# Performance work log

Hardware: AMD Instinct MI355X
Metric: run time of the kernel (lower is better)

Reference implementation:

```python
import jax, jax.numpy as jnp
import numpy as np

K = 128        # numClass
PUW = 1.0      # puW from __init__
EPS = 0.01     # the +0.01 clamp inside log(1 - p + 0.01)


def setup_inputs() -> dict:
    key = jax.random.key(0)
    k1, k2, k3 = jax.random.split(key, 3)
    N = 262144
    outputs = jax.random.normal(k1, (N, K), dtype=jnp.float32)
    # labels in [0, K]; label == K means 'unlabeled' (goes to U set)
    labels = jax.random.randint(k2, (N,), 0, K + 1, dtype=jnp.int64)
    priorlist = jax.random.uniform(k3, (K,), dtype=jnp.float32)
    indexlist = jnp.arange(32, dtype=jnp.int64)  # the 32 labeled classes
    return {"outputs": outputs, "labels": labels,
            "priorlist": priorlist, "indexlist": indexlist}


def reference(outputs, labels, priorlist, indexlist):
    outputs = outputs.astype(jnp.float32)
    s = jax.nn.softmax(outputs, axis=1)                      # [N, K]

    maskP = (labels <= K - 1)                                # positive (labeled)
    maskU = jnp.logical_not(maskP)                           # unlabeled
    fP = maskP.astype(jnp.float32)
    fU = maskU.astype(jnp.float32)
    nP = jnp.maximum(jnp.float32(1.0), fP.sum())
    nU = jnp.maximum(jnp.float32(1.0), fU.sum())

    neglog = -jnp.log(1.0 - s + EPS)                         # [N, K]
    sumU = jnp.sum(neglog * fU[:, None], axis=0)             # [K] sums over U rows
    sumP = jnp.sum(neglog * fP[:, None], axis=0)             # [K] sums over P rows

    L = indexlist.shape[0]
    in_idx = jnp.zeros((K,), dtype=bool).at[indexlist].set(True)

    # classes in indexlist: pu3; classes not in indexlist: pu1
    pu3 = jnp.sum(jnp.where(in_idx, sumU, 0.0)) / nU / L
    pu1 = (jnp.sum(jnp.where(in_idx, 0.0, sumP))
           * priorlist[indexlist[0]] / nP / (K - L))

    # pu2: per positive sample, -log(1 - p[label] + eps) * prior[label]
    lab_c = jnp.clip(labels, 0, K - 1)
    gathered = jnp.take_along_axis(neglog, lab_c[:, None], axis=1)[:, 0]
    pu2 = jnp.sum(gathered * priorlist[lab_c] * fP) / nP

    PULoss = pu3 + pu1 - pu2

    # mean cross-entropy over positive samples only
    logp = jax.nn.log_softmax(outputs, axis=1)
    ce_per = -jnp.take_along_axis(logp, lab_c[:, None], axis=1)[:, 0]
    crossloss = jnp.sum(ce_per * fP) / nP

    objective = crossloss
    return (objective, PULoss * PUW, crossloss)
```

## Files before the change

kernel.cpp:

```cpp
#include <hip/hip_runtime.h>
#include <math.h>

#define KCLS 128

__global__ __launch_bounds__(256) void pu_main(
    const float* __restrict__ outp, const int* __restrict__ labels,
    const int* __restrict__ idxlist, const float* __restrict__ prior,
    double* __restrict__ acc, int N, int L)
{
    __shared__ __align__(16) float s_notin[KCLS];
    __shared__ __align__(16) float s_prior[KCLS];
    const int tid = threadIdx.x;
    if (tid < KCLS) { s_prior[tid] = prior[tid]; s_notin[tid] = 1.0f; }
    __syncthreads();
    if (tid < L) s_notin[idxlist[tid]] = 0.0f;
    __syncthreads();

    const int lane  = tid & 63;
    const int wave  = tid >> 6;
    const int half  = lane >> 5;
    const int hlane = lane & 31;
    const int globalWave = blockIdx.x * (blockDim.x >> 6) + wave;
    const int numWaves   = gridDim.x * (blockDim.x >> 6);

    const float4 nm4 = ((const float4*)s_notin)[hlane];
    const float4 in4 = make_float4(1.f - nm4.x, 1.f - nm4.y,
                                   1.f - nm4.z, 1.f - nm4.w);
    const float4 pr4 = ((const float4*)s_prior)[hlane];

    float aU = 0.f, aP = 0.f, aPu2 = 0.f, aCE = 0.f, cP = 0.f, cU = 0.f;

    const int npairs = (N + 1) >> 1;
    for (int pair = globalWave; pair < npairs; pair += numWaves) {
        const int row   = pair * 2 + half;
        const bool valid = (row < N);
        const int  rl    = valid ? row : (N - 1);

        const float4 o4 = ((const float4*)(outp + (size_t)rl * KCLS))[hlane];
        const int  lab  = labels[rl];
        const bool isP  = (lab < KCLS);
        const int  labc = isP ? lab : (KCLS - 1);

        const float e0 = __expf(o4.x), e1 = __expf(o4.y),
                    e2 = __expf(o4.z), e3 = __expf(o4.w);
        float psum = (e0 + e1) + (e2 + e3);
        #pragma unroll
        for (int off = 16; off; off >>= 1)
            psum += __shfl_xor(psum, off);
        const float inv = __builtin_amdgcn_rcpf(psum);

        const float s0 = e0 * inv, s1 = e1 * inv, s2 = e2 * inv, s3 = e3 * inv;
        const float nl0 = -__logf((1.0f - s0) + 0.01f);
        const float nl1 = -__logf((1.0f - s1) + 0.01f);
        const float nl2 = -__logf((1.0f - s2) + 0.01f);
        const float nl3 = -__logf((1.0f - s3) + 0.01f);

        const float vP = (valid && isP)  ? 1.f : 0.f;
        const float vU = (valid && !isP) ? 1.f : 0.f;

        aP += vP * ((nl0 * nm4.x + nl1 * nm4.y) + (nl2 * nm4.z + nl3 * nm4.w));
        aU += vU * ((nl0 * in4.x + nl1 * in4.y) + (nl2 * in4.z + nl3 * in4.w));

        if ((labc >> 2) == hlane) {
            const int sub = labc & 3;
            const float olab = (sub == 0) ? o4.x : (sub == 1) ? o4.y : (sub == 2) ? o4.z : o4.w;
            const float nll  = (sub == 0) ? nl0  : (sub == 1) ? nl1  : (sub == 2) ? nl2  : nl3;
            const float prl  = (sub == 0) ? pr4.x : (sub == 1) ? pr4.y : (sub == 2) ? pr4.z : pr4.w;
            aPu2 += vP * nll * prl;
            aCE  += vP * (__logf(psum) - olab);
        }
        if (hlane == 0) { cP += vP; cU += vU; }
    }

    #pragma unroll
    for (int off = 32; off; off >>= 1) {
        aU   += __shfl_xor(aU, off);
        aP   += __shfl_xor(aP, off);
        aPu2 += __shfl_xor(aPu2, off);
        aCE  += __shfl_xor(aCE, off);
        cP   += __shfl_xor(cP, off);
        cU   += __shfl_xor(cU, off);
    }

    __shared__ float s_red[4][6];
    if (lane == 0) {
        s_red[wave][0] = aU;  s_red[wave][1] = aP;   s_red[wave][2] = aPu2;
        s_red[wave][3] = aCE; s_red[wave][4] = cP;   s_red[wave][5] = cU;
    }
    __syncthreads();
    if (tid < 6) {
        float t = 0.f;
        const int nw = blockDim.x >> 6;
        for (int w = 0; w < nw; ++w) t += s_red[w][tid];
        atomicAdd(&acc[tid * 8], (double)t);
    }
}

__global__ void pu_final(const double* __restrict__ acc,
                         const float* __restrict__ prior,
                         const int* __restrict__ idxlist,
                         float* __restrict__ out, int L)
{
    const double aU   = acc[0 * 8];
    const double aP   = acc[1 * 8];
    const double aPu2 = acc[2 * 8];
    const double aCE  = acc[3 * 8];
    const double cP   = acc[4 * 8];
    const double cU   = acc[5 * 8];
    const double nP = cP > 1.0 ? cP : 1.0;
    const double nU = cU > 1.0 ? cU : 1.0;

    const double pu3 = aU / nU / (double)L;
    const double pu1 = aP * (double)prior[idxlist[0]] / nP / (double)(KCLS - L);
    const double pu2 = aPu2 / nP;
    const double ce  = aCE / nP;

    out[0] = (float)ce;
    out[1] = (float)(pu3 + pu1 - pu2);
    out[2] = (float)ce;
}

extern "C" void kernel_launch(void* const* d_in, const int* in_sizes, int n_in,
                              void* d_out, int out_size, void* d_ws, size_t ws_size,
                              hipStream_t stream)
{
    const float* outp   = (const float*)d_in[0];
    const int*   labels = (const int*)d_in[1];
    const float* prior  = (const float*)d_in[2];
    const int*   idxl   = (const int*)d_in[3];
    const int N = in_sizes[1];
    const int L = in_sizes[3];

    double* acc = (double*)d_ws;
    hipMemsetAsync(d_ws, 0, 48 * sizeof(double), stream);

    pu_main<<<1024, 256, 0, stream>>>(outp, labels, idxl, prior, acc, N, L);
    pu_final<<<1, 1, 0, stream>>>(acc, prior, idxl, (float*)d_out, L);
}
```

Measured before the change: 213.6 us.

## Unroll row loop by two and replace double atomics with per-block partials

```diff
diff --git a/kernel.cpp b/kernel.cpp
--- a/kernel.cpp
+++ b/kernel.cpp
@@ -2,11 +2,13 @@
 #include <math.h>
 
 #define KCLS 128
+#define NBLK 1024
+
 
 __global__ __launch_bounds__(256) void pu_main(
     const float* __restrict__ outp, const int* __restrict__ labels,
     const int* __restrict__ idxlist, const float* __restrict__ prior,
-    double* __restrict__ acc, int N, int L)
+    float* __restrict__ part, int N, int L)
 {
     __shared__ __align__(16) float s_notin[KCLS];
     __shared__ __align__(16) float s_prior[KCLS];
@@ -21,7 +23,7 @@
     const int half  = lane >> 5;
     const int hlane = lane & 31;
     const int globalWave = blockIdx.x * (blockDim.x >> 6) + wave;
-    const int numWaves   = gridDim.x * (blockDim.x >> 6);
+    const int numWaves   = NBLK * (256 >> 6);
 
     const float4 nm4 = ((const float4*)s_notin)[hlane];
     const float4 in4 = make_float4(1.f - nm4.x, 1.f - nm4.y,
@@ -30,14 +32,7 @@
 
     float aU = 0.f, aP = 0.f, aPu2 = 0.f, aCE = 0.f, cP = 0.f, cU = 0.f;
 
-    const int npairs = (N + 1) >> 1;
-    for (int pair = globalWave; pair < npairs; pair += numWaves) {
-        const int row   = pair * 2 + half;
-        const bool valid = (row < N);
-        const int  rl    = valid ? row : (N - 1);
-
-        const float4 o4 = ((const float4*)(outp + (size_t)rl * KCLS))[hlane];
-        const int  lab  = labels[rl];
+    auto process = [&](float4 o4, int lab) {
         const bool isP  = (lab < KCLS);
         const int  labc = isP ? lab : (KCLS - 1);
 
@@ -55,8 +50,8 @@
         const float nl2 = -__logf((1.0f - s2) + 0.01f);
         const float nl3 = -__logf((1.0f - s3) + 0.01f);
 
-        const float vP = (valid && isP)  ? 1.f : 0.f;
-        const float vU = (valid && !isP) ? 1.f : 0.f;
+        const float vP = isP ? 1.f : 0.f;
+        const float vU = 1.f - vP;
 
         aP += vP * ((nl0 * nm4.x + nl1 * nm4.y) + (nl2 * nm4.z + nl3 * nm4.w));
         aU += vU * ((nl0 * in4.x + nl1 * in4.y) + (nl2 * in4.z + nl3 * in4.w));
@@ -70,6 +65,24 @@
             aCE  += vP * (__logf(psum) - olab);
         }
         if (hlane == 0) { cP += vP; cU += vU; }
+    };
+
+    const int npairs = N >> 1;
+    int pair = globalWave;
+    for (; pair + numWaves < npairs; pair += 2 * numWaves) {
+        const int rowA = pair * 2 + half;
+        const int rowB = (pair + numWaves) * 2 + half;
+        const float4 oA = ((const float4*)(outp + (size_t)rowA * KCLS))[hlane];
+        const int    lA = labels[rowA];
+        const float4 oB = ((const float4*)(outp + (size_t)rowB * KCLS))[hlane];
+        const int    lB = labels[rowB];
+        process(oA, lA);
+        process(oB, lB);
+    }
+    for (; pair < npairs; pair += numWaves) {
+        const int row = pair * 2 + half;
+        const float4 o = ((const float4*)(outp + (size_t)row * KCLS))[hlane];
+        process(o, labels[row]);
     }
 
     #pragma unroll
@@ -89,35 +102,54 @@
     }
     __syncthreads();
     if (tid < 6) {
-        float t = 0.f;
-        const int nw = blockDim.x >> 6;
-        for (int w = 0; w < nw; ++w) t += s_red[w][tid];
-        atomicAdd(&acc[tid * 8], (double)t);
+        float t = s_red[0][tid] + s_red[1][tid] + s_red[2][tid] + s_red[3][tid];
+        part[tid * NBLK + blockIdx.x] = t;
     }
 }
 
-__global__ void pu_final(const double* __restrict__ acc,
-                         const float* __restrict__ prior,
-                         const int* __restrict__ idxlist,
-                         float* __restrict__ out, int L)
+__global__ __launch_bounds__(256) void pu_final(
+    const float* __restrict__ part, const float* __restrict__ prior,
+    const int* __restrict__ idxlist, float* __restrict__ out, int L)
 {
-    const double aU   = acc[0 * 8];
-    const double aP   = acc[1 * 8];
-    const double aPu2 = acc[2 * 8];
-    const double aCE  = acc[3 * 8];
-    const double cP   = acc[4 * 8];
-    const double cU   = acc[5 * 8];
-    const double nP = cP > 1.0 ? cP : 1.0;
-    const double nU = cU > 1.0 ? cU : 1.0;
+    const int tid  = threadIdx.x;
+    const int lane = tid & 63;
+    const int wave = tid >> 6;
 
-    const double pu3 = aU / nU / (double)L;
-    const double pu1 = aP * (double)prior[idxlist[0]] / nP / (double)(KCLS - L);
-    const double pu2 = aPu2 / nP;
-    const double ce  = aCE / nP;
+    double loc[6] = {0, 0, 0, 0, 0, 0};
+    for (int b = tid; b < NBLK; b += 256) {
+        #pragma unroll
+        for (int c = 0; c < 6; ++c) loc[c] += (double)part[c * NBLK + b];
+    }
+    #pragma unroll
+    for (int off = 32; off; off >>= 1) {
+        #pragma unroll
+        for (int c = 0; c < 6; ++c) loc[c] += __shfl_xor(loc[c], off);
+    }
+    __shared__ double s_red[4][6];
+    if (lane == 0) {
+        #pragma unroll
+        for (int c = 0; c < 6; ++c) s_red[wave][c] = loc[c];
+    }
+    __syncthreads();
+    if (tid == 0) {
+        const double aU   = s_red[0][0] + s_red[1][0] + s_red[2][0] + s_red[3][0];
+        const double aP   = s_red[0][1] + s_red[1][1] + s_red[2][1] + s_red[3][1];
+        const double aPu2 = s_red[0][2] + s_red[1][2] + s_red[2][2] + s_red[3][2];
+        const double aCE  = s_red[0][3] + s_red[1][3] + s_red[2][3] + s_red[3][3];
+        const double cP   = s_red[0][4] + s_red[1][4] + s_red[2][4] + s_red[3][4];
+        const double cU   = s_red[0][5] + s_red[1][5] + s_red[2][5] + s_red[3][5];
+        const double nP = cP > 1.0 ? cP : 1.0;
+        const double nU = cU > 1.0 ? cU : 1.0;
 
-    out[0] = (float)ce;
-    out[1] = (float)(pu3 + pu1 - pu2);
-    out[2] = (float)ce;
+        const double pu3 = aU / nU / (double)L;
+        const double pu1 = aP * (double)prior[idxlist[0]] / nP / (double)(KCLS - L);
+        const double pu2 = aPu2 / nP;
+        const double ce  = aCE / nP;
+
+        out[0] = (float)ce;
+        out[1] = (float)(pu3 + pu1 - pu2);
+        out[2] = (float)ce;
+    }
 }
 
 extern "C" void kernel_launch(void* const* d_in, const int* in_sizes, int n_in,
@@ -131,9 +163,8 @@
     const int N = in_sizes[1];
     const int L = in_sizes[3];
 
-    double* acc = (double*)d_ws;
-    hipMemsetAsync(d_ws, 0, 48 * sizeof(double), stream);
+    float* part = (float*)d_ws;
 
-    pu_main<<<1024, 256, 0, stream>>>(outp, labels, idxl, prior, acc, N, L);
-    pu_final<<<1, 1, 0, stream>>>(acc, prior, idxl, (float*)d_out, L);
+    pu_main<<<NBLK, 256, 0, stream>>>(outp, labels, idxl, prior, part, N, L);
+    pu_final<<<1, 256, 0, stream>>>(part, prior, idxl, (float*)d_out, L);
 }
```

Measured after the change: 196.2 us. 8.2% less time.
